# Kernel tuning notes

Measured on AMD Instinct MI355X. Metric: run time of the kernel, lower is better.

## Reference

```python
import jax, jax.numpy as jnp
import numpy as np

B, S, D, H = 2, 2048, 1024, 16
HD = D // H
MAX_BIAS = 8.0


def setup_inputs() -> dict:
    key = jax.random.key(0)
    ks = jax.random.split(key, 5)
    sc = 1.0 / np.sqrt(D)
    return {
        "x": jax.random.normal(ks[0], (B, S, D), jnp.float32),
        "Wq": jax.random.normal(ks[1], (D, D), jnp.float32) * sc,
        "bq": jnp.zeros((D,), jnp.float32),
        "Wk": jax.random.normal(ks[2], (D, D), jnp.float32) * sc,
        "bk": jnp.zeros((D,), jnp.float32),
        "Wv": jax.random.normal(ks[3], (D, D), jnp.float32) * sc,
        "bv": jnp.zeros((D,), jnp.float32),
        "Wo": jax.random.normal(ks[4], (D, D), jnp.float32) * sc,
        "bo": jnp.zeros((D,), jnp.float32),
    }


def _alibi_bias(T, Sk, dtype):
    # slopes: (2 ** (-max_bias / H)) ** (h + 1)
    slopes = (2.0 ** (-MAX_BIAS / H)) ** (jnp.arange(1, H + 1, dtype=dtype))
    qpos = jnp.arange(T)[:, None]
    kpos = jnp.arange(Sk)[None, :]
    rel = -jnp.abs(kpos - qpos).astype(dtype)            # (T, S)
    return slopes[:, None, None] * rel[None]              # (H, T, S)


def reference(x, Wq, bq, Wk, bk, Wv, bv, Wo, bo):
    Bb, Ss, Dd = x.shape
    q = (x @ Wq + bq).reshape(Bb, Ss, H, HD)
    k = (x @ Wk + bk).reshape(Bb, Ss, H, HD)
    v = (x @ Wv + bv).reshape(Bb, Ss, H, HD)
    scores = jnp.einsum("bthd,bshd->bhts", q, k) / jnp.sqrt(jnp.asarray(HD, x.dtype))
    alibi = _alibi_bias(Ss, Ss, x.dtype)                  # (H, T, S)
    causal = jnp.triu(jnp.ones((Ss, Ss), bool), 1)        # key > query -> masked
    scores = scores + alibi[None]
    scores = jnp.where(causal[None, None], -jnp.inf, scores)
    attn = jax.nn.softmax(scores, axis=-1)
    out = jnp.einsum("bhts,bshd->bthd", attn, v).reshape(Bb, Ss, Dd)
    return out @ Wo + bo
```

## Files before the change

### kernel.cpp

```cpp
#include <hip/hip_runtime.h>
#include <hip/hip_bf16.h>

constexpr int B_ = 2, S_ = 2048, D_ = 1024, H_ = 16, HD_ = 64;

typedef __attribute__((ext_vector_type(8))) short bf16x8;
typedef __attribute__((ext_vector_type(4))) short bf16x4;
typedef __attribute__((ext_vector_type(4))) float f32x4;

#if __has_builtin(__builtin_amdgcn_mfma_f32_16x16x16bf16_1k)
#define MFMA16(acc, a, b) \
    (acc) = __builtin_amdgcn_mfma_f32_16x16x16bf16_1k((a), (b), (acc), 0, 0, 0)
#else
#define MFMA16(acc, a, b) \
    asm("v_mfma_f32_16x16x16_bf16 %0, %1, %2, %0" : "+v"(acc) : "v"(a), "v"(b))
#endif

typedef __attribute__((address_space(1))) const unsigned char ga_t;
typedef __attribute__((address_space(3))) unsigned char la_t;
__device__ __forceinline__ void gload_lds16(const void* g, void* l) {
    __builtin_amdgcn_global_load_lds((ga_t*)g, (la_t*)l, 16, 0, 0);
}

__device__ __forceinline__ short f2bf(float x) {
    __hip_bfloat16 h = __float2bfloat16(x);
    return *reinterpret_cast<short*>(&h);
}

__global__ void f32_to_bf16_vec(const float* __restrict__ in,
                                __hip_bfloat16* __restrict__ out, int n) {
    int i = (blockIdx.x * 256 + threadIdx.x) * 4;
    if (i >= n) return;
    float4 v = *reinterpret_cast<const float4*>(in + i);
    union { ushort4 u; __hip_bfloat16 h[4]; } pk;
    pk.h[0] = __float2bfloat16(v.x);
    pk.h[1] = __float2bfloat16(v.y);
    pk.h[2] = __float2bfloat16(v.z);
    pk.h[3] = __float2bfloat16(v.w);
    *reinterpret_cast<ushort4*>(out + i) = pk.u;
}

__global__ void transpose4_f32_to_bf16(const float* __restrict__ w0,
                                       const float* __restrict__ w1,
                                       const float* __restrict__ w2,
                                       const float* __restrict__ w3,
                                       __hip_bfloat16* __restrict__ d0,
                                       __hip_bfloat16* __restrict__ d1,
                                       __hip_bfloat16* __restrict__ d2,
                                       __hip_bfloat16* __restrict__ d3) {
    __shared__ float tile[32][33];
    const int z = blockIdx.z;
    const float* src = z == 0 ? w0 : z == 1 ? w1 : z == 2 ? w2 : w3;
    __hip_bfloat16* dst = z == 0 ? d0 : z == 1 ? d1 : z == 2 ? d2 : d3;
    const int bx = blockIdx.x * 32;
    const int by = blockIdx.y * 32;
    const int c = threadIdx.x & 31;
    const int r0 = threadIdx.x >> 5;
#pragma unroll
    for (int p = 0; p < 4; ++p) {
        int r = r0 + p * 8;
        tile[r][c] = src[(size_t)(by + r) * D_ + bx + c];
    }
    __syncthreads();
#pragma unroll
    for (int p = 0; p < 4; ++p) {
        int r = r0 + p * 8;
        dst[(size_t)(bx + r) * D_ + by + c] = __float2bfloat16(tile[c][r]);
    }
}

__global__ void concat_bias(const float* __restrict__ bq, const float* __restrict__ bk,
                            const float* __restrict__ bv, float* __restrict__ dst) {
    int i = blockIdx.x * 256 + threadIdx.x;
    float v = (i < 1024) ? bq[i] : (i < 2048) ? bk[i - 1024] : bv[i - 2048];
    dst[i] = v;
}

template <bool OUT_F32>
__launch_bounds__(256)
__global__ void gemm_bt_kernel(const __hip_bfloat16* __restrict__ A,
                               const __hip_bfloat16* __restrict__ Bt,
                               const float* __restrict__ bias,
                               void* __restrict__ Cout,
                               int M, int N, int K) {
    constexpr int BM = 128, BN = 128, BK = 64;
    __shared__ __hip_bfloat16 As[BM][BK];
    __shared__ __hip_bfloat16 Bs[BN][BK];

    const int tid = threadIdx.x;
    const int lane = tid & 63;
    const int w = tid >> 6;
    const int wr = w >> 1, wc = w & 1;
    const int g = lane >> 4;
    const int lc = lane & 15;
    const int m0 = blockIdx.x * BM;
    const int n0 = blockIdx.y * BN;

    const int srow = tid >> 3;
    const int sc0 = (tid & 7) * 8;
    const int scol = sc0 ^ ((srow & 7) << 3);

    f32x4 acc[4][4] = {};

    for (int k0 = 0; k0 < K; k0 += BK) {
#pragma unroll
        for (int p = 0; p < 4; ++p) {
            int r = p * 32 + srow;
            gload_lds16(&A[(size_t)(m0 + r) * K + k0 + scol], &As[r][sc0]);
            gload_lds16(&Bt[(size_t)(n0 + r) * K + k0 + scol], &Bs[r][sc0]);
        }
        __syncthreads();
#pragma unroll
        for (int kk = 0; kk < 2; ++kk) {
            bf16x8 af[4], bfr[4];
#pragma unroll
            for (int mi = 0; mi < 4; ++mi) {
                int row = wr * 64 + mi * 16 + lc;
                af[mi] = *reinterpret_cast<const bf16x8*>(
                    &As[row][(kk * 32 + g * 8) ^ ((row & 7) << 3)]);
            }
#pragma unroll
            for (int ni = 0; ni < 4; ++ni) {
                int row = wc * 64 + ni * 16 + lc;
                bfr[ni] = *reinterpret_cast<const bf16x8*>(
                    &Bs[row][(kk * 32 + g * 8) ^ ((row & 7) << 3)]);
            }
#pragma unroll
            for (int mi = 0; mi < 4; ++mi)
#pragma unroll
                for (int ni = 0; ni < 4; ++ni)
                    acc[mi][ni] = __builtin_amdgcn_mfma_f32_16x16x32_bf16(af[mi], bfr[ni], acc[mi][ni], 0, 0, 0);
        }
        __syncthreads();
    }

#pragma unroll
    for (int mi = 0; mi < 4; ++mi)
#pragma unroll
        for (int r = 0; r < 4; ++r) {
            int row = m0 + wr * 64 + mi * 16 + g * 4 + r;
#pragma unroll
            for (int ni = 0; ni < 4; ++ni) {
                int col = n0 + wc * 64 + ni * 16 + lc;
                float v = acc[mi][ni][r] + bias[col];
                if (OUT_F32)
                    ((float*)Cout)[(size_t)row * N + col] = v;
                else
                    ((__hip_bfloat16*)Cout)[(size_t)row * N + col] = __float2bfloat16(v);
            }
        }
}

__launch_bounds__(256)
__global__ void attn_kernel(const __hip_bfloat16* __restrict__ qkv,
                            __hip_bfloat16* __restrict__ outb) {
    __shared__ __hip_bfloat16 Ks[64][64];
    __shared__ __hip_bfloat16 Vt[64][72];

    const int tid = threadIdx.x;
    const int lane = tid & 63;
    const int w = tid >> 6;
    const int bh = blockIdx.y;
    const int b = bh >> 4, h = bh & 15;
    const int g = lane >> 4;
    const int lc = lane & 15;
    const int lq = w * 16 + lc;

    const float slope = exp2f(-0.5f * (float)(h + 1));

    const size_t rowstride = 3 * D_;
    const size_t base = (size_t)b * S_ * rowstride + h * HD_;

    const int srow = tid >> 3;
    const int sc0 = (tid & 7) * 8;
    const int kscol = sc0 ^ ((srow & 7) << 3);
    const int vwsz = (tid & 7) << 3;

#pragma unroll 1
    for (int phase = 0; phase < 2; ++phase) {
        const int qt = phase == 0 ? (31 - blockIdx.x) : blockIdx.x;
        const int qg = qt * 64 + lq;

        bf16x8 aq[2];
#pragma unroll
        for (int kk = 0; kk < 2; ++kk)
            aq[kk] = *reinterpret_cast<const bf16x8*>(
                &qkv[base + (size_t)qg * rowstride + kk * 32 + g * 8]);

        f32x4 o[4] = {};
        float m_run = -3e38f, l_run = 0.f;

        for (int kt = 0; kt <= qt; ++kt) {
#pragma unroll
            for (int p = 0; p < 2; ++p) {
                int r = p * 32 + srow;
                gload_lds16(&qkv[base + (size_t)(kt * 64 + r) * rowstride + D_ + kscol],
                            &Ks[r][sc0]);
            }
#pragma unroll
            for (int p = 0; p < 2; ++p) {
                int r = p * 32 + srow;
                uint4 vv = *reinterpret_cast<const uint4*>(
                    &qkv[base + (size_t)(kt * 64 + r) * rowstride + 2 * D_ + sc0]);
                const __hip_bfloat16* ve = reinterpret_cast<const __hip_bfloat16*>(&vv);
#pragma unroll
                for (int j = 0; j < 8; ++j)
                    Vt[sc0 + j][r ^ vwsz] = ve[j];
            }
            __syncthreads();

            f32x4 s[4] = {};
#pragma unroll
            for (int ni = 0; ni < 4; ++ni)
#pragma unroll
                for (int kk = 0; kk < 2; ++kk) {
                    int row = ni * 16 + lc;
                    bf16x8 kf = *reinterpret_cast<const bf16x8*>(
                        &Ks[row][(kk * 32 + g * 8) ^ ((row & 7) << 3)]);
                    s[ni] = __builtin_amdgcn_mfma_f32_16x16x32_bf16(kf, aq[kk], s[ni], 0, 0, 0);
                }

            const bool diag = (kt == qt);
            const float dlt = (float)(kt * 64 - qg);
            float v[16];
#pragma unroll
            for (int ni = 0; ni < 4; ++ni)
#pragma unroll
                for (int r = 0; r < 4; ++r) {
                    const int koff = 16 * ni + 4 * g + r;
                    float t = fmaf(s[ni][r], 0.125f, slope * (dlt + (float)koff));
                    if (diag && koff > lq) t = -3e38f;
                    v[ni * 4 + r] = t;
                }

            float t8[8], t4[4];
#pragma unroll
            for (int i = 0; i < 8; ++i) t8[i] = fmaxf(v[i], v[i + 8]);
#pragma unroll
            for (int i = 0; i < 4; ++i) t4[i] = fmaxf(t8[i], t8[i + 4]);
            float rm = fmaxf(fmaxf(t4[0], t4[1]), fmaxf(t4[2], t4[3]));
            rm = fmaxf(rm, __shfl_xor(rm, 16, 64));
            rm = fmaxf(rm, __shfl_xor(rm, 32, 64));

            const float mnew = fmaxf(m_run, rm);
            const float alpha = __expf(m_run - mnew);
            m_run = mnew;

#pragma unroll
            for (int i = 0; i < 16; ++i) v[i] = __expf(v[i] - mnew);
            float s8[8], s4[4];
#pragma unroll
            for (int i = 0; i < 8; ++i) s8[i] = v[i] + v[i + 8];
#pragma unroll
            for (int i = 0; i < 4; ++i) s4[i] = s8[i] + s8[i + 4];
            float rs = (s4[0] + s4[1]) + (s4[2] + s4[3]);
            rs += __shfl_xor(rs, 16, 64);
            rs += __shfl_xor(rs, 32, 64);
            l_run = l_run * alpha + rs;

            bf16x4 pb[4];
#pragma unroll
            for (int ni = 0; ni < 4; ++ni) {
#pragma unroll
                for (int r = 0; r < 4; ++r) {
                    o[ni][r] *= alpha;
                    pb[ni][r] = f2bf(v[ni * 4 + r]);
                }
            }

#pragma unroll
            for (int oi = 0; oi < 4; ++oi) {
                const int row = oi * 16 + lc;
                const int key = ((row >> 3) & 7) << 3;
#pragma unroll
                for (int ni = 0; ni < 4; ++ni) {
                    bf16x4 vf = *reinterpret_cast<const bf16x4*>(
                        &Vt[row][(ni * 16 + 4 * g) ^ key]);
                    MFMA16(o[oi], vf, pb[ni]);
                }
            }
            __syncthreads();
        }

        const float inv = 1.0f / l_run;
#pragma unroll
        for (int oi = 0; oi < 4; ++oi) {
            union { ushort4 u; short s[4]; } pk;
#pragma unroll
            for (int r = 0; r < 4; ++r) pk.s[r] = f2bf(o[oi][r] * inv);
            *reinterpret_cast<ushort4*>(
                &outb[(size_t)(b * S_ + qg) * D_ + h * HD_ + oi * 16 + 4 * g]) = pk.u;
        }
    }
}

extern "C" void kernel_launch(void* const* d_in, const int* in_sizes, int n_in,
                              void* d_out, int out_size, void* d_ws, size_t ws_size,
                              hipStream_t stream) {
    const float* x  = (const float*)d_in[0];
    const float* Wq = (const float*)d_in[1];
    const float* bq = (const float*)d_in[2];
    const float* Wk = (const float*)d_in[3];
    const float* bk = (const float*)d_in[4];
    const float* Wv = (const float*)d_in[5];
    const float* bv = (const float*)d_in[6];
    const float* Wo = (const float*)d_in[7];
    const float* bo = (const float*)d_in[8];

    char* ws = (char*)d_ws;
    __hip_bfloat16* xb    = (__hip_bfloat16*)(ws);
    __hip_bfloat16* Wqkvt = (__hip_bfloat16*)(ws + (size_t)(8u  << 20));
    __hip_bfloat16* Wot   = (__hip_bfloat16*)(ws + (size_t)(14u << 20));
    __hip_bfloat16* qkv   = (__hip_bfloat16*)(ws + (size_t)(16u << 20));
    __hip_bfloat16* attnb = (__hip_bfloat16*)(ws + (size_t)(40u << 20));
    float* biasf          = (float*)(ws + (size_t)(48u << 20));

    const int nX = B_ * S_ * D_;

    f32_to_bf16_vec<<<4096, 256, 0, stream>>>(x, xb, nX);
    transpose4_f32_to_bf16<<<dim3(32, 32, 4), 256, 0, stream>>>(
        Wq, Wk, Wv, Wo, Wqkvt, Wqkvt + D_ * D_, Wqkvt + 2 * D_ * D_, Wot);
    concat_bias<<<12, 256, 0, stream>>>(bq, bk, bv, biasf);

    gemm_bt_kernel<false><<<dim3(32, 24), 256, 0, stream>>>(
        xb, Wqkvt, biasf, qkv, B_ * S_, 3 * D_, D_);

    attn_kernel<<<dim3(S_ / 128, B_ * H_), 256, 0, stream>>>(qkv, attnb);

    gemm_bt_kernel<true><<<dim3(32, 8), 256, 0, stream>>>(
        attnb, Wot, bo, (float*)d_out, B_ * S_, D_, D_);
}
```

Baseline: 215.4 us.

## Double-buffer K/V tiles in attention, one q-tile per block, narrower output GEMM tile

The attention kernel now double-buffers its K and V tiles in LDS, prefetching the next tile while the current one is processed, and drops one barrier per iteration. It launches one 64-row query tile per block, heaviest tiles first, instead of pairing tiles for causal balance. Softmax moves to exp2 with log2e folded into the scale and a precomputed ALiBi offset. The output projection GEMM uses a 64-wide N tile so it launches more blocks across CUs. The cost is double the LDS per attention block, more registers held for the prefetch, and possible load imbalance without tile pairing.

Measured after the change: 209.5 us. -2.7%, faster.

```diff
diff --git a/kernel.cpp b/kernel.cpp
--- a/kernel.cpp
+++ b/kernel.cpp
@@ -75,16 +75,17 @@
     dst[i] = v;
 }
 
-template <bool OUT_F32>
+template <bool OUT_F32, int BN_>
 __launch_bounds__(256)
 __global__ void gemm_bt_kernel(const __hip_bfloat16* __restrict__ A,
                                const __hip_bfloat16* __restrict__ Bt,
                                const float* __restrict__ bias,
                                void* __restrict__ Cout,
                                int M, int N, int K) {
-    constexpr int BM = 128, BN = 128, BK = 64;
+    constexpr int BM = 128, BK = 64;
+    constexpr int NI = BN_ / 32;
     __shared__ __hip_bfloat16 As[BM][BK];
-    __shared__ __hip_bfloat16 Bs[BN][BK];
+    __shared__ __hip_bfloat16 Bs[BN_][BK];
 
     const int tid = threadIdx.x;
     const int lane = tid & 63;
@@ -93,25 +94,29 @@
     const int g = lane >> 4;
     const int lc = lane & 15;
     const int m0 = blockIdx.x * BM;
-    const int n0 = blockIdx.y * BN;
+    const int n0 = blockIdx.y * BN_;
 
     const int srow = tid >> 3;
     const int sc0 = (tid & 7) * 8;
     const int scol = sc0 ^ ((srow & 7) << 3);
 
-    f32x4 acc[4][4] = {};
+    f32x4 acc[4][NI] = {};
 
     for (int k0 = 0; k0 < K; k0 += BK) {
 #pragma unroll
         for (int p = 0; p < 4; ++p) {
             int r = p * 32 + srow;
             gload_lds16(&A[(size_t)(m0 + r) * K + k0 + scol], &As[r][sc0]);
+        }
+#pragma unroll
+        for (int p = 0; p < BN_ / 32; ++p) {
+            int r = p * 32 + srow;
             gload_lds16(&Bt[(size_t)(n0 + r) * K + k0 + scol], &Bs[r][sc0]);
         }
         __syncthreads();
 #pragma unroll
         for (int kk = 0; kk < 2; ++kk) {
-            bf16x8 af[4], bfr[4];
+            bf16x8 af[4], bfr[NI];
 #pragma unroll
             for (int mi = 0; mi < 4; ++mi) {
                 int row = wr * 64 + mi * 16 + lc;
@@ -119,15 +124,15 @@
                     &As[row][(kk * 32 + g * 8) ^ ((row & 7) << 3)]);
             }
 #pragma unroll
-            for (int ni = 0; ni < 4; ++ni) {
-                int row = wc * 64 + ni * 16 + lc;
+            for (int ni = 0; ni < NI; ++ni) {
+                int row = wc * (BN_ / 2) + ni * 16 + lc;
                 bfr[ni] = *reinterpret_cast<const bf16x8*>(
                     &Bs[row][(kk * 32 + g * 8) ^ ((row & 7) << 3)]);
             }
 #pragma unroll
             for (int mi = 0; mi < 4; ++mi)
 #pragma unroll
-                for (int ni = 0; ni < 4; ++ni)
+                for (int ni = 0; ni < NI; ++ni)
                     acc[mi][ni] = __builtin_amdgcn_mfma_f32_16x16x32_bf16(af[mi], bfr[ni], acc[mi][ni], 0, 0, 0);
         }
         __syncthreads();
@@ -139,8 +144,8 @@
         for (int r = 0; r < 4; ++r) {
             int row = m0 + wr * 64 + mi * 16 + g * 4 + r;
 #pragma unroll
-            for (int ni = 0; ni < 4; ++ni) {
-                int col = n0 + wc * 64 + ni * 16 + lc;
+            for (int ni = 0; ni < NI; ++ni) {
+                int col = n0 + wc * (BN_ / 2) + ni * 16 + lc;
                 float v = acc[mi][ni][r] + bias[col];
                 if (OUT_F32)
                     ((float*)Cout)[(size_t)row * N + col] = v;
@@ -153,19 +158,21 @@
 __launch_bounds__(256)
 __global__ void attn_kernel(const __hip_bfloat16* __restrict__ qkv,
                             __hip_bfloat16* __restrict__ outb) {
-    __shared__ __hip_bfloat16 Ks[64][64];
-    __shared__ __hip_bfloat16 Vt[64][72];
+    __shared__ __hip_bfloat16 Ks[2][64][64];
+    __shared__ __hip_bfloat16 Vt[2][64][72];
 
     const int tid = threadIdx.x;
     const int lane = tid & 63;
     const int w = tid >> 6;
-    const int bh = blockIdx.y;
+    const int bh = blockIdx.x;
     const int b = bh >> 4, h = bh & 15;
     const int g = lane >> 4;
     const int lc = lane & 15;
     const int lq = w * 16 + lc;
 
-    const float slope = exp2f(-0.5f * (float)(h + 1));
+    constexpr float LOG2E = 1.44269504088896f;
+    constexpr float SC = 0.125f * LOG2E;
+    const float slope2 = exp2f(-0.5f * (float)(h + 1)) * LOG2E;
 
     const size_t rowstride = 3 * D_;
     const size_t base = (size_t)b * S_ * rowstride + h * HD_;
@@ -175,121 +182,145 @@
     const int kscol = sc0 ^ ((srow & 7) << 3);
     const int vwsz = (tid & 7) << 3;
 
-#pragma unroll 1
-    for (int phase = 0; phase < 2; ++phase) {
-        const int qt = phase == 0 ? (31 - blockIdx.x) : blockIdx.x;
-        const int qg = qt * 64 + lq;
-
-        bf16x8 aq[2];
-#pragma unroll
-        for (int kk = 0; kk < 2; ++kk)
-            aq[kk] = *reinterpret_cast<const bf16x8*>(
-                &qkv[base + (size_t)qg * rowstride + kk * 32 + g * 8]);
-
-        f32x4 o[4] = {};
-        float m_run = -3e38f, l_run = 0.f;
-
-        for (int kt = 0; kt <= qt; ++kt) {
+    const int qt = 31 - blockIdx.y;
+    const int qg = qt * 64 + lq;
+
+    bf16x8 aq[2];
+#pragma unroll
+    for (int kk = 0; kk < 2; ++kk)
+        aq[kk] = *reinterpret_cast<const bf16x8*>(
+            &qkv[base + (size_t)qg * rowstride + kk * 32 + g * 8]);
+
+    float ab[16];
+#pragma unroll
+    for (int ni = 0; ni < 4; ++ni)
+#pragma unroll
+        for (int r = 0; r < 4; ++r)
+            ab[ni * 4 + r] = slope2 * (float)(16 * ni + 4 * g + r);
+
+    f32x4 o[4] = {};
+    float m_run = -3e38f, l_run = 0.f;
+
+#pragma unroll
+    for (int p = 0; p < 2; ++p) {
+        int r = p * 32 + srow;
+        gload_lds16(&qkv[base + (size_t)r * rowstride + D_ + kscol], &Ks[0][r][sc0]);
+        uint4 vv = *reinterpret_cast<const uint4*>(
+            &qkv[base + (size_t)r * rowstride + 2 * D_ + sc0]);
+        const __hip_bfloat16* ve = reinterpret_cast<const __hip_bfloat16*>(&vv);
+#pragma unroll
+        for (int j = 0; j < 8; ++j)
+            Vt[0][sc0 + j][r ^ vwsz] = ve[j];
+    }
+    __syncthreads();
+
+    int cur = 0;
+    for (int kt = 0; kt <= qt; ++kt) {
+        const bool havepre = (kt < qt);
+        uint4 vpre[2];
+        if (havepre) {
 #pragma unroll
             for (int p = 0; p < 2; ++p) {
                 int r = p * 32 + srow;
-                gload_lds16(&qkv[base + (size_t)(kt * 64 + r) * rowstride + D_ + kscol],
-                            &Ks[r][sc0]);
-            }
+                gload_lds16(&qkv[base + (size_t)((kt + 1) * 64 + r) * rowstride + D_ + kscol],
+                            &Ks[cur ^ 1][r][sc0]);
+                vpre[p] = *reinterpret_cast<const uint4*>(
+                    &qkv[base + (size_t)((kt + 1) * 64 + r) * rowstride + 2 * D_ + sc0]);
+            }
+        }
+
+        f32x4 s[4] = {};
+#pragma unroll
+        for (int ni = 0; ni < 4; ++ni)
+#pragma unroll
+            for (int kk = 0; kk < 2; ++kk) {
+                int row = ni * 16 + lc;
+                bf16x8 kf = *reinterpret_cast<const bf16x8*>(
+                    &Ks[cur][row][(kk * 32 + g * 8) ^ ((row & 7) << 3)]);
+                s[ni] = __builtin_amdgcn_mfma_f32_16x16x32_bf16(kf, aq[kk], s[ni], 0, 0, 0);
+            }
+
+        const bool diag = (kt == qt);
+        const float b0 = slope2 * (float)(kt * 64 - qg);
+        float v[16];
+#pragma unroll
+        for (int ni = 0; ni < 4; ++ni)
+#pragma unroll
+            for (int r = 0; r < 4; ++r) {
+                const int koff = 16 * ni + 4 * g + r;
+                float t = fmaf(s[ni][r], SC, b0 + ab[ni * 4 + r]);
+                if (diag && koff > lq) t = -3e38f;
+                v[ni * 4 + r] = t;
+            }
+
+        float t8[8], t4[4];
+#pragma unroll
+        for (int i = 0; i < 8; ++i) t8[i] = fmaxf(v[i], v[i + 8]);
+#pragma unroll
+        for (int i = 0; i < 4; ++i) t4[i] = fmaxf(t8[i], t8[i + 4]);
+        float rm = fmaxf(fmaxf(t4[0], t4[1]), fmaxf(t4[2], t4[3]));
+        rm = fmaxf(rm, __shfl_xor(rm, 16, 64));
+        rm = fmaxf(rm, __shfl_xor(rm, 32, 64));
+
+        const float mnew = fmaxf(m_run, rm);
+        const float alpha = exp2f(m_run - mnew);
+        m_run = mnew;
+
+#pragma unroll
+        for (int i = 0; i < 16; ++i) v[i] = exp2f(v[i] - mnew);
+        float s8[8], s4[4];
+#pragma unroll
+        for (int i = 0; i < 8; ++i) s8[i] = v[i] + v[i + 8];
+#pragma unroll
+        for (int i = 0; i < 4; ++i) s4[i] = s8[i] + s8[i + 4];
+        float rs = (s4[0] + s4[1]) + (s4[2] + s4[3]);
+        rs += __shfl_xor(rs, 16, 64);
+        rs += __shfl_xor(rs, 32, 64);
+        l_run = l_run * alpha + rs;
+
+        bf16x4 pb[4];
+#pragma unroll
+        for (int ni = 0; ni < 4; ++ni)
+#pragma unroll
+            for (int r = 0; r < 4; ++r) {
+                o[ni][r] *= alpha;
+                pb[ni][r] = f2bf(v[ni * 4 + r]);
+            }
+
+#pragma unroll
+        for (int oi = 0; oi < 4; ++oi) {
+            const int row = oi * 16 + lc;
+            const int key = ((row >> 3) & 7) << 3;
+#pragma unroll
+            for (int ni = 0; ni < 4; ++ni) {
+                bf16x4 vf = *reinterpret_cast<const bf16x4*>(
+                    &Vt[cur][row][(ni * 16 + 4 * g) ^ key]);
+                MFMA16(o[oi], vf, pb[ni]);
+            }
+        }
+
+        if (havepre) {
 #pragma unroll
             for (int p = 0; p < 2; ++p) {
                 int r = p * 32 + srow;
-                uint4 vv = *reinterpret_cast<const uint4*>(
-                    &qkv[base + (size_t)(kt * 64 + r) * rowstride + 2 * D_ + sc0]);
-                const __hip_bfloat16* ve = reinterpret_cast<const __hip_bfloat16*>(&vv);
+                const __hip_bfloat16* ve = reinterpret_cast<const __hip_bfloat16*>(&vpre[p]);
 #pragma unroll
                 for (int j = 0; j < 8; ++j)
-                    Vt[sc0 + j][r ^ vwsz] = ve[j];
-            }
-            __syncthreads();
-
-            f32x4 s[4] = {};
-#pragma unroll
-            for (int ni = 0; ni < 4; ++ni)
-#pragma unroll
-                for (int kk = 0; kk < 2; ++kk) {
-                    int row = ni * 16 + lc;
-                    bf16x8 kf = *reinterpret_cast<const bf16x8*>(
-                        &Ks[row][(kk * 32 + g * 8) ^ ((row & 7) << 3)]);
-                    s[ni] = __builtin_amdgcn_mfma_f32_16x16x32_bf16(kf, aq[kk], s[ni], 0, 0, 0);
-                }
-
-            const bool diag = (kt == qt);
-            const float dlt = (float)(kt * 64 - qg);
-            float v[16];
-#pragma unroll
-            for (int ni = 0; ni < 4; ++ni)
-#pragma unroll
-                for (int r = 0; r < 4; ++r) {
-                    const int koff = 16 * ni + 4 * g + r;
-                    float t = fmaf(s[ni][r], 0.125f, slope * (dlt + (float)koff));
-                    if (diag && koff > lq) t = -3e38f;
-                    v[ni * 4 + r] = t;
-                }
-
-            float t8[8], t4[4];
-#pragma unroll
-            for (int i = 0; i < 8; ++i) t8[i] = fmaxf(v[i], v[i + 8]);
-#pragma unroll
-            for (int i = 0; i < 4; ++i) t4[i] = fmaxf(t8[i], t8[i + 4]);
-            float rm = fmaxf(fmaxf(t4[0], t4[1]), fmaxf(t4[2], t4[3]));
-            rm = fmaxf(rm, __shfl_xor(rm, 16, 64));
-            rm = fmaxf(rm, __shfl_xor(rm, 32, 64));
-
-            const float mnew = fmaxf(m_run, rm);
-            const float alpha = __expf(m_run - mnew);
-            m_run = mnew;
-
-#pragma unroll
-            for (int i = 0; i < 16; ++i) v[i] = __expf(v[i] - mnew);
-            float s8[8], s4[4];
-#pragma unroll
-            for (int i = 0; i < 8; ++i) s8[i] = v[i] + v[i + 8];
-#pragma unroll
-            for (int i = 0; i < 4; ++i) s4[i] = s8[i] + s8[i + 4];
-            float rs = (s4[0] + s4[1]) + (s4[2] + s4[3]);
-            rs += __shfl_xor(rs, 16, 64);
-            rs += __shfl_xor(rs, 32, 64);
-            l_run = l_run * alpha + rs;
-
-            bf16x4 pb[4];
-#pragma unroll
-            for (int ni = 0; ni < 4; ++ni) {
-#pragma unroll
-                for (int r = 0; r < 4; ++r) {
-                    o[ni][r] *= alpha;
-                    pb[ni][r] = f2bf(v[ni * 4 + r]);
-                }
-            }
-
-#pragma unroll
-            for (int oi = 0; oi < 4; ++oi) {
-                const int row = oi * 16 + lc;
-                const int key = ((row >> 3) & 7) << 3;
-#pragma unroll
-                for (int ni = 0; ni < 4; ++ni) {
-                    bf16x4 vf = *reinterpret_cast<const bf16x4*>(
-                        &Vt[row][(ni * 16 + 4 * g) ^ key]);
-                    MFMA16(o[oi], vf, pb[ni]);
-                }
-            }
-            __syncthreads();
-        }
-
-        const float inv = 1.0f / l_run;
-#pragma unroll
-        for (int oi = 0; oi < 4; ++oi) {
-            union { ushort4 u; short s[4]; } pk;
-#pragma unroll
-            for (int r = 0; r < 4; ++r) pk.s[r] = f2bf(o[oi][r] * inv);
-            *reinterpret_cast<ushort4*>(
-                &outb[(size_t)(b * S_ + qg) * D_ + h * HD_ + oi * 16 + 4 * g]) = pk.u;
-        }
+                    Vt[cur ^ 1][sc0 + j][r ^ vwsz] = ve[j];
+            }
+        }
+        __syncthreads();
+        cur ^= 1;
+    }
+
+    const float inv = 1.0f / l_run;
+#pragma unroll
+    for (int oi = 0; oi < 4; ++oi) {
+        union { ushort4 u; short s[4]; } pk;
+#pragma unroll
+        for (int r = 0; r < 4; ++r) pk.s[r] = f2bf(o[oi][r] * inv);
+        *reinterpret_cast<ushort4*>(
+            &outb[(size_t)(b * S_ + qg) * D_ + h * HD_ + oi * 16 + 4 * g]) = pk.u;
     }
 }
 
@@ -321,11 +352,11 @@
         Wq, Wk, Wv, Wo, Wqkvt, Wqkvt + D_ * D_, Wqkvt + 2 * D_ * D_, Wot);
     concat_bias<<<12, 256, 0, stream>>>(bq, bk, bv, biasf);
 
-    gemm_bt_kernel<false><<<dim3(32, 24), 256, 0, stream>>>(
+    gemm_bt_kernel<false, 128><<<dim3(32, 24), 256, 0, stream>>>(
         xb, Wqkvt, biasf, qkv, B_ * S_, 3 * D_, D_);
 
-    attn_kernel<<<dim3(S_ / 128, B_ * H_), 256, 0, stream>>>(qkv, attnb);
-
-    gemm_bt_kernel<true><<<dim3(32, 8), 256, 0, stream>>>(
+    attn_kernel<<<dim3(B_ * H_, S_ / 64), 256, 0, stream>>>(qkv, attnb);
+
+    gemm_bt_kernel<true, 64><<<dim3(32, 16), 256, 0, stream>>>(
         attnb, Wot, bo, (float*)d_out, B_ * S_, D_, D_);
 }
```
